# Optimization experiments

Hardware: AMD Instinct MI355X
Metric: run time of the kernel (lower is better)

The kernel has to match this reference:

```python
import jax, jax.numpy as jnp
import numpy as np

N = 2048          # n_network_nodes
E = 10240         # n_interactions (avg degree ~5)
B = 512           # samples
MAX_STEPS = 60    # bionet_params['max_steps']
LEAK = 0.01       # bionet_params['leak']


def mml(x, leak):
    """Michaelis-Menten-like activation (LEMBAS 'MML'):
    leak*x for x<0, x for 0<=x<0.5, 1 - 0.25/x for x>=0.5."""
    xs = jnp.maximum(x, 0.5)  # safe denominator
    return jnp.where(x < 0.0, leak * x,
                     jnp.where(x < 0.5, x, 1.0 - 0.25 / xs))


def setup_inputs() -> dict:
    key = jax.random.key(0)
    k1, k2, k3, k4, k5 = jax.random.split(key, 5)
    # sparse signaling graph: edge_list = (targets, sources)
    tgt = jax.random.randint(k1, (E,), 0, N)
    src = jax.random.randint(k2, (E,), 0, N)
    # initialize_weight_values: 0.1 + 0.1*rand, negate inhibiting edges
    wv = 0.1 + 0.1 * jax.random.uniform(k3, (E,), dtype=jnp.float32)
    inhibiting = jax.random.uniform(k4, (E,)) < 0.3
    wv = jnp.where(inhibiting, -wv, wv)
    # scatter into dense masked adjacency (off-edge entries are exactly 0,
    # matching weights.masked_fill_(mask, 0.0) in forward)
    weights = jnp.zeros((N, N), dtype=jnp.float32).at[tgt, src].set(wv)
    bias = 0.001 * jnp.ones((N, 1), dtype=jnp.float32)
    X_full = jax.random.uniform(k5, (B, N), dtype=jnp.float32)  # scaled ligand inputs
    return {"X_full": X_full, "weights": weights, "bias": bias}


def reference(X_full, weights, bias):
    # X_bias: (N, B) = X_full.T + bias
    X_bias = X_full.T + bias
    X0 = jnp.zeros_like(X_bias)

    def step(X, _):
        Xn = mml(weights @ X + X_bias, LEAK)
        return Xn, None

    Xf, _ = jax.lax.scan(step, X0, None, length=MAX_STEPS)
    return Xf.T  # (B, N)
```

## Files before the change

kernel.cpp:

```cpp
#include <hip/hip_runtime.h>


#define NN 2048
#define STEPS 60
#define LEAKV 0.01f
#define EMAX 10240
#define TPB 1024
#define SPB 2
#define NB 64
#define EPT 12
#define BUF1 16384
#define CEPS 1e-6f

typedef float vf2 __attribute__((ext_vector_type(2)));

__device__ __forceinline__ float mml_f(float x) {
  if (x < 0.0f)      return LEAKV * x;
  else if (x < 0.5f) return x;
  else               return 1.0f - 0.25f / x;
}

__global__ __launch_bounds__(64) void count_row(const float* __restrict__ W,
                                                int* __restrict__ cnt) {
  const int n = blockIdx.x, lane = threadIdx.x;
  int c = 0;
  for (int c0 = 0; c0 < NN; c0 += 64) {
    float w = W[n * NN + c0 + lane];
    c += __popcll(__ballot(w != 0.0f));
  }
  if (lane == 0) cnt[n] = c;
}

__global__ __launch_bounds__(1024) void plan(const int* __restrict__ cnt,
                                             int* __restrict__ tb,
                                             int* __restrict__ tmid,
                                             int* __restrict__ pa,
                                             int* __restrict__ pb,
                                             int* __restrict__ rowstart) {
  __shared__ int sperm[NN];
  __shared__ int sc[2][1024];
  __shared__ int bases[NB];
  const int t = threadIdx.x;

  if (t < NB) bases[t] = 0;
  __syncthreads();
  const int d0 = min(cnt[t], NB - 1), d1 = min(cnt[t + 1024], NB - 1);
  atomicAdd(&bases[d0], 1);
  atomicAdd(&bases[d1], 1);
  __syncthreads();
  if (t == 0) {
    int acc = 0;
    for (int i = 0; i < NB; ++i) { int h = bases[i]; bases[i] = acc; acc += h; }
  }
  __syncthreads();
  sperm[atomicAdd(&bases[d0], 1)] = t;
  sperm[atomicAdd(&bases[d1], 1)] = t + 1024;
  __syncthreads();

  const int nA = sperm[t], nB = sperm[2047 - t];
  const int dA = cnt[nA], dB = cnt[nB];
  sc[0][t] = dA + dB;
  __syncthreads();
  int p = 0;
  for (int off = 1; off < 1024; off <<= 1) {
    sc[p ^ 1][t] = sc[p][t] + (t >= off ? sc[p][t - off] : 0);
    __syncthreads();
    p ^= 1;
  }
  const int b0 = sc[p][t] - (dA + dB);
  tb[t] = b0;
  tmid[t] = b0 + dA;
  pa[t] = nA;
  pb[t] = nB;
  if (t == 1023) tb[1024] = sc[p][t];
  rowstart[nA] = b0;
  rowstart[nB] = b0 + dA;
}

__global__ __launch_bounds__(64) void fill2(const float* __restrict__ W,
                                            const int* __restrict__ rowstart,
                                            uint2* __restrict__ e2) {
  const int n = blockIdx.x, lane = threadIdx.x;
  const int b = rowstart[n];
  int off = 0;
  for (int c0 = 0; c0 < NN; c0 += 64) {
    float w = W[n * NN + c0 + lane];
    unsigned long long m = __ballot(w != 0.0f);
    if (w != 0.0f) {
      int e = b + off + __popcll(m & ((1ull << lane) - 1ull));
      e2[e] = make_uint2(__float_as_uint(w), (unsigned)(c0 + lane));
    }
    off += __popcll(m);
  }
}

__global__ __launch_bounds__(TPB, 4) void sim(const float* __restrict__ Xfull,
                                              const float* __restrict__ bias,
                                              const uint2* __restrict__ e2,
                                              const int* __restrict__ tb,
                                              const int* __restrict__ tmid,
                                              const int* __restrict__ pa,
                                              const int* __restrict__ pb,
                                              float* __restrict__ out) {
  __shared__ float2 X[2][NN];
  __shared__ int chg[32];
  char* Xb = (char*)&X[0][0];
  const int t  = (int)threadIdx.x;
  const int s0 = (int)blockIdx.x * SPB;

  const int eA0 = tb[t], eA1 = tmid[t], eB1 = tb[t + 1];
  const int spill0 = eA0 + EPT;
  const int nA = pa[t], nB = pb[t];
  const int wA_off = nA * 8, wB_off = nB * 8;

  float wA[EPT], wB[EPT];
  int boff[EPT];
#pragma unroll
  for (int k = 0; k < EPT; ++k) {
    const int idx = eA0 + k;
    const bool val = idx < eB1;
    const uint2 en = e2[val ? idx : eA0];
    const float wv = val ? __uint_as_float(en.x) : 0.0f;
    const bool isA = idx < eA1;
    wA[k] = isA ? wv : 0.0f;
    wB[k] = isA ? 0.0f : wv;
    boff[k] = val ? (int)(en.y * 8u) : 0;
  }

  const vf2 xbA = {Xfull[(size_t)s0 * NN + nA] + bias[nA],
                   Xfull[(size_t)(s0 + 1) * NN + nA] + bias[nA]};
  const vf2 xbB = {Xfull[(size_t)s0 * NN + nB] + bias[nB],
                   Xfull[(size_t)(s0 + 1) * NN + nB] + bias[nB]};

  if (t < 32) chg[t] = 0;
  *(vf2*)(Xb + wA_off) = (vf2){mml_f(xbA.x), mml_f(xbA.y)};
  *(vf2*)(Xb + wB_off) = (vf2){mml_f(xbB.x), mml_f(xbB.y)};
  __syncthreads();

  vf2 yA, yB;

#define STEP_C(SRCOFF, DSTOFF, CHK, CI)                                      \
  {                                                                          \
    vf2 aA = xbA, aB = xbB;                                                  \
    _Pragma("unroll")                                                        \
    for (int k = 0; k < EPT; ++k) {                                          \
      const vf2 v = *(const vf2*)(Xb + (SRCOFF) + boff[k]);                  \
      aA += wA[k] * v;                                                       \
      aB += wB[k] * v;                                                       \
    }                                                                        \
    for (int e = spill0; e < eB1; ++e) {                                     \
      const uint2 en = e2[e];                                                \
      const float w = __uint_as_float(en.x);                                 \
      const vf2 v = *(const vf2*)(Xb + (SRCOFF) + (int)(en.y * 8u));         \
      if (e < eA1) { aA.x += w * v.x; aA.y += w * v.y; }                     \
      else         { aB.x += w * v.x; aB.y += w * v.y; }                     \
    }                                                                        \
    yA = (vf2){mml_f(aA.x), mml_f(aA.y)};                                    \
    yB = (vf2){mml_f(aB.x), mml_f(aB.y)};                                    \
    *(vf2*)(Xb + (DSTOFF) + wA_off) = yA;                                    \
    *(vf2*)(Xb + (DSTOFF) + wB_off) = yB;                                    \
    if (CHK) {                                                               \
      const float d = fmaxf(fmaxf(fabsf(yA.x - pA.x), fabsf(yA.y - pA.y)),   \
                            fmaxf(fabsf(yB.x - pB.x), fabsf(yB.y - pB.y)));  \
      if (__ballot(d > CEPS)) { if ((t & 63) == 0) chg[CI] = 1; }            \
    }                                                                        \
    __syncthreads();                                                         \
  }

  vf2 pA, pB;
  STEP_C(0, BUF1, 0, 0);
  for (int i = 0; i < (STEPS - 2) / 2; ++i) {
    STEP_C(BUF1, 0, 0, 0);
    pA = yA; pB = yB;
    STEP_C(0, BUF1, 1, i);
    if (chg[i] == 0) break;
  }
#undef STEP_C

  out[(size_t)s0 * NN + nA]       = yA.x;
  out[(size_t)(s0 + 1) * NN + nA] = yA.y;
  out[(size_t)s0 * NN + nB]       = yB.x;
  out[(size_t)(s0 + 1) * NN + nB] = yB.y;
}

extern "C" void kernel_launch(void* const* d_in, const int* in_sizes, int n_in,
                              void* d_out, int out_size, void* d_ws, size_t ws_size,
                              hipStream_t stream) {
  const float* Xfull = (const float*)d_in[0];
  const float* W     = (const float*)d_in[1];
  const float* bias  = (const float*)d_in[2];
  float* out = (float*)d_out;

  char* ws = (char*)d_ws;
  uint2* e2     = (uint2*)ws;                           ws += (size_t)EMAX * 8;
  int* cnt      = (int*)ws;                             ws += (size_t)NN * 4;
  int* tb       = (int*)ws;                             ws += (size_t)1025 * 4;
  int* tmid     = (int*)ws;                             ws += (size_t)1024 * 4;
  int* pa       = (int*)ws;                             ws += (size_t)1024 * 4;
  int* pb       = (int*)ws;                             ws += (size_t)1024 * 4;
  int* rowstart = (int*)ws;

  const int B = in_sizes[0] / NN;

  count_row<<<NN, 64, 0, stream>>>(W, cnt);
  plan<<<1, 1024, 0, stream>>>(cnt, tb, tmid, pa, pb, rowstart);
  fill2<<<NN, 64, 0, stream>>>(W, rowstart, e2);
  sim<<<B / SPB, TPB, 0, stream>>>(Xfull, bias, e2, tb, tmid, pa, pb, out);
}
```

Baseline: 43.85 us.

## Merge count and fill passes over W; check convergence every step

```diff
diff --git a/kernel.cpp b/kernel.cpp
--- a/kernel.cpp
+++ b/kernel.cpp
@@ -9,6 +9,7 @@
 #define SPB 2
 #define NB 64
 #define EPT 12
+#define PAD 32
 #define BUF1 16384
 #define CEPS 1e-6f
 
@@ -20,23 +21,32 @@
   else               return 1.0f - 0.25f / x;
 }
 
-__global__ __launch_bounds__(64) void count_row(const float* __restrict__ W,
+__global__ __launch_bounds__(64) void scan_fill(const float* __restrict__ W,
+                                                uint2* __restrict__ pgpad,
                                                 int* __restrict__ cnt) {
   const int n = blockIdx.x, lane = threadIdx.x;
-  int c = 0;
+  int base = 0;
   for (int c0 = 0; c0 < NN; c0 += 64) {
     float w = W[n * NN + c0 + lane];
-    c += __popcll(__ballot(w != 0.0f));
-  }
-  if (lane == 0) cnt[n] = c;
-}
-
-__global__ __launch_bounds__(1024) void plan(const int* __restrict__ cnt,
-                                             int* __restrict__ tb,
-                                             int* __restrict__ tmid,
-                                             int* __restrict__ pa,
-                                             int* __restrict__ pb,
-                                             int* __restrict__ rowstart) {
+    unsigned long long m = __ballot(w != 0.0f);
+    if (w != 0.0f) {
+      int slot = base + __popcll(m & ((1ull << lane) - 1ull));
+      if (slot < PAD)
+        pgpad[n * PAD + slot] = make_uint2(__float_as_uint(w),
+                                           (unsigned)(c0 + lane));
+    }
+    base += __popcll(m);
+  }
+  if (lane == 0) cnt[n] = base < PAD ? base : PAD;
+}
+
+__global__ __launch_bounds__(1024) void plan2(const int* __restrict__ cnt,
+                                              const uint2* __restrict__ pgpad,
+                                              uint2* __restrict__ e2,
+                                              int* __restrict__ tb,
+                                              int* __restrict__ tmid,
+                                              int* __restrict__ pa,
+                                              int* __restrict__ pb) {
   __shared__ int sperm[NN];
   __shared__ int sc[2][1024];
   __shared__ int bases[NB];
@@ -73,25 +83,9 @@
   pa[t] = nA;
   pb[t] = nB;
   if (t == 1023) tb[1024] = sc[p][t];
-  rowstart[nA] = b0;
-  rowstart[nB] = b0 + dA;
-}
-
-__global__ __launch_bounds__(64) void fill2(const float* __restrict__ W,
-                                            const int* __restrict__ rowstart,
-                                            uint2* __restrict__ e2) {
-  const int n = blockIdx.x, lane = threadIdx.x;
-  const int b = rowstart[n];
-  int off = 0;
-  for (int c0 = 0; c0 < NN; c0 += 64) {
-    float w = W[n * NN + c0 + lane];
-    unsigned long long m = __ballot(w != 0.0f);
-    if (w != 0.0f) {
-      int e = b + off + __popcll(m & ((1ull << lane) - 1ull));
-      e2[e] = make_uint2(__float_as_uint(w), (unsigned)(c0 + lane));
-    }
-    off += __popcll(m);
-  }
+
+  for (int k = 0; k < dA; ++k) e2[b0 + k] = pgpad[nA * PAD + k];
+  for (int k = 0; k < dB; ++k) e2[b0 + dA + k] = pgpad[nB * PAD + k];
 }
 
 __global__ __launch_bounds__(TPB, 4) void sim(const float* __restrict__ Xfull,
@@ -103,7 +97,7 @@
                                               const int* __restrict__ pb,
                                               float* __restrict__ out) {
   __shared__ float2 X[2][NN];
-  __shared__ int chg[32];
+  __shared__ int chg[64];
   char* Xb = (char*)&X[0][0];
   const int t  = (int)threadIdx.x;
   const int s0 = (int)blockIdx.x * SPB;
@@ -132,12 +126,12 @@
   const vf2 xbB = {Xfull[(size_t)s0 * NN + nB] + bias[nB],
                    Xfull[(size_t)(s0 + 1) * NN + nB] + bias[nB]};
 
-  if (t < 32) chg[t] = 0;
+  if (t < 64) chg[t] = 0;
   *(vf2*)(Xb + wA_off) = (vf2){mml_f(xbA.x), mml_f(xbA.y)};
   *(vf2*)(Xb + wB_off) = (vf2){mml_f(xbB.x), mml_f(xbB.y)};
   __syncthreads();
 
-  vf2 yA, yB;
+  vf2 yA, yB, pA, pB;
 
 #define STEP_C(SRCOFF, DSTOFF, CHK, CI)                                      \
   {                                                                          \
@@ -167,13 +161,15 @@
     __syncthreads();                                                         \
   }
 
-  vf2 pA, pB;
   STEP_C(0, BUF1, 0, 0);
+  pA = yA; pB = yB;
   for (int i = 0; i < (STEPS - 2) / 2; ++i) {
-    STEP_C(BUF1, 0, 0, 0);
+    STEP_C(BUF1, 0, 1, 2 * i);
+    if (chg[2 * i] == 0) break;
     pA = yA; pB = yB;
-    STEP_C(0, BUF1, 1, i);
-    if (chg[i] == 0) break;
+    STEP_C(0, BUF1, 1, 2 * i + 1);
+    if (chg[2 * i + 1] == 0) break;
+    pA = yA; pB = yB;
   }
 #undef STEP_C
 
@@ -192,18 +188,17 @@
   float* out = (float*)d_out;
 
   char* ws = (char*)d_ws;
-  uint2* e2     = (uint2*)ws;                           ws += (size_t)EMAX * 8;
-  int* cnt      = (int*)ws;                             ws += (size_t)NN * 4;
-  int* tb       = (int*)ws;                             ws += (size_t)1025 * 4;
-  int* tmid     = (int*)ws;                             ws += (size_t)1024 * 4;
-  int* pa       = (int*)ws;                             ws += (size_t)1024 * 4;
-  int* pb       = (int*)ws;                             ws += (size_t)1024 * 4;
-  int* rowstart = (int*)ws;
+  uint2* pgpad = (uint2*)ws;                            ws += (size_t)NN * PAD * 8;
+  uint2* e2    = (uint2*)ws;                            ws += (size_t)EMAX * 8;
+  int* cnt     = (int*)ws;                              ws += (size_t)NN * 4;
+  int* tb      = (int*)ws;                              ws += (size_t)1025 * 4;
+  int* tmid    = (int*)ws;                              ws += (size_t)1024 * 4;
+  int* pa      = (int*)ws;                              ws += (size_t)1024 * 4;
+  int* pb      = (int*)ws;
 
   const int B = in_sizes[0] / NN;
 
-  count_row<<<NN, 64, 0, stream>>>(W, cnt);
-  plan<<<1, 1024, 0, stream>>>(cnt, tb, tmid, pa, pb, rowstart);
-  fill2<<<NN, 64, 0, stream>>>(W, rowstart, e2);
+  scan_fill<<<NN, 64, 0, stream>>>(W, pgpad, cnt);
+  plan2<<<1, 1024, 0, stream>>>(cnt, pgpad, e2, tb, tmid, pa, pb);
   sim<<<B / SPB, TPB, 0, stream>>>(Xfull, bias, e2, tb, tmid, pa, pb, out);
 }
```

After: 53.32 us. +21.6%, slower.
